# Optimization experiments

Measured on AMD Instinct MI355X. Metric: run time of the kernel, lower is better.

## Reference

```python
import jax, jax.numpy as jnp
import numpy as np
from jax import lax

EPS = 1e-5
B, T, IN, H, D = 16, 512, 128, 256, 8


def setup_inputs() -> dict:
    key = jax.random.key(0)
    ks = jax.random.split(key, 9)
    s = 0.05  # small init to keep tanh unsaturated
    f32 = jnp.float32
    return {
        "y": jax.random.normal(ks[0], (B, T, IN), f32),
        "W_ih": jax.random.normal(ks[1], (H, IN), f32) * s,
        "W_hh": jax.random.normal(ks[2], (H, H), f32) * s,
        "b_ih": jax.random.normal(ks[3], (H,), f32) * s,
        "b_hh": jax.random.normal(ks[4], (H,), f32) * s,
        "W_mean": jax.random.normal(ks[5], (D, H), f32) * s,
        "b_mean": jax.random.normal(ks[6], (D,), f32) * s,
        "W_bd": jax.random.normal(ks[7], (2 * D, H), f32) * s,
        "b_bd": jax.random.normal(ks[8], (2 * D,), f32) * s,
    }


def _forward(y, W_ih, W_hh, b_ih, b_hh, W_mean, b_mean, W_bd, b_bd):
    # --- single-layer unidirectional tanh RNN (torch nn.RNN, batch_first) ---
    x_proj = jnp.einsum("bti,hi->bth", y, W_ih) + b_ih  # [B,T,H]

    def step(h, xt):
        h_new = jnp.tanh(xt + h @ W_hh.T + b_hh)
        return h_new, h_new

    h0 = jnp.zeros((y.shape[0], W_hh.shape[0]), y.dtype)
    _, hs = lax.scan(step, h0, jnp.swapaxes(x_proj, 0, 1))  # [T,B,H]
    enc = jnp.swapaxes(hs, 0, 1)  # [B,T,H]

    mean = enc @ W_mean.T + b_mean  # [B,T,D]
    bd = enc @ W_bd.T + b_bd        # [B,T,2D]

    d = mean.shape[-1]
    t = bd.shape[1]
    diag_e = bd[:, :, :d]        # [B,T,D]  main-diag factor elems
    off_e = bd[:, :-1, d:]       # [B,T-1,D] super-diag factor elems

    a2 = diag_e ** 2
    b2 = jnp.concatenate([jnp.zeros_like(off_e[:, :1]), off_e ** 2], axis=1)  # [B,T,D]
    ab = diag_e[:, :-1] * off_e  # [B,T-1,D]

    main = jnp.swapaxes(a2 + b2, 1, 2) + EPS  # [B,D,T]  (eps*I folded into diag)
    supd = jnp.swapaxes(ab, 1, 2)             # [B,D,T-1]

    i = jnp.arange(t)
    j = jnp.arange(t - 1)
    prec = jnp.zeros((bd.shape[0], d, t, t), bd.dtype)  # [B,D,T,T]
    prec = prec.at[:, :, i, i].set(main)
    prec = prec.at[:, :, j, j + 1].set(supd)
    prec = prec.at[:, :, j + 1, j].set(supd)
    return mean, prec


def reference(y, W_ih, W_hh, b_ih, b_hh, W_mean, b_mean, W_bd, b_bd):
    # Returns the parameters of the D per-dim MultivariateNormal posteriors:
    # mean [B,T,D] and tridiagonal precision matrices [B,D,T,T].
    return _forward(y, W_ih, W_hh, b_ih, b_hh, W_mean, b_mean, W_bd, b_bd)
```

## Files before the change

kernel.cpp:

```cpp
#include <hip/hip_runtime.h>
#include <math.h>

#define BB 16
#define TT 512
#define IND 128
#define HH 256
#define DD 8
#define EPSF 1e-5f

typedef _Float16 h2_t __attribute__((ext_vector_type(2)));
typedef float f32x4 __attribute__((ext_vector_type(4)));

__device__ __forceinline__ float fast_tanh(float x) {
    x = fminf(fmaxf(x, -15.f), 15.f);
    const float e = __expf(2.f * x);
    return __fdividef(e - 1.f, e + 1.f);
}

__device__ __forceinline__ float dpp_xor1(float x) {
    int i = __builtin_bit_cast(int, x);
    i = __builtin_amdgcn_update_dpp(i, i, 0xB1, 0xF, 0xF, true);
    return __builtin_bit_cast(float, i);
}
__device__ __forceinline__ float dpp_xor2(float x) {
    int i = __builtin_bit_cast(int, x);
    i = __builtin_amdgcn_update_dpp(i, i, 0x4E, 0xF, 0xF, true);
    return __builtin_bit_cast(float, i);
}

__global__ __launch_bounds__(512, 4) void xproj_kernel(
    const float* __restrict__ y, const float* __restrict__ W_ih,
    const float* __restrict__ b_ih, const float* __restrict__ b_hh,
    float* __restrict__ xp)
{
    __shared__ __align__(16) float ylds[IND];
    const int tid = threadIdx.x;
    const int j = tid >> 1;
    const int k4 = (tid & 1) * 4;

    float4 w[16];
    const float* wr = W_ih + (size_t)j * IND + k4;
#pragma unroll
    for (int i = 0; i < 16; ++i) w[i] = *(const float4*)(wr + i * 8);
#pragma unroll
    for (int i = 0; i < 16; ++i)
        asm volatile("" : "+v"(w[i].x), "+v"(w[i].y), "+v"(w[i].z), "+v"(w[i].w));
    const float bias = b_ih[j] + b_hh[j];

    const int row0 = blockIdx.x * 16;
    for (int r = 0; r < 16; ++r) {
        const int row = row0 + r;
        if (tid < IND / 4) ((float4*)ylds)[tid] = ((const float4*)(y + (size_t)row * IND))[tid];
        __syncthreads();
        float a0 = 0.f, a1 = 0.f, a2 = 0.f, a3 = 0.f;
#pragma unroll
        for (int i = 0; i < 16; ++i) {
            const float4 hv = *(const float4*)(ylds + i * 8 + k4);
            a0 = fmaf(hv.x, w[i].x, a0);
            a1 = fmaf(hv.y, w[i].y, a1);
            a2 = fmaf(hv.z, w[i].z, a2);
            a3 = fmaf(hv.w, w[i].w, a3);
        }
        float acc = (a0 + a1) + (a2 + a3);
        acc += __shfl_xor(acc, 1);
        if ((tid & 1) == 0) xp[(size_t)row * HH + j] = acc + bias;
        __syncthreads();
    }
}

__global__ __launch_bounds__(512, 2) void scan_fill_kernel(
    const float* __restrict__ xp, const float* __restrict__ W_hh,
    float* __restrict__ enc, float* __restrict__ prec)
{
    if (blockIdx.x >= BB) {
        const size_t n4 = (size_t)BB * DD * TT * TT / 4;
        const f32x4 z = {0.f, 0.f, 0.f, 0.f};
        f32x4* p4 = (f32x4*)prec;
        size_t idx = (size_t)(blockIdx.x - BB) * blockDim.x + threadIdx.x;
        const size_t stride = (size_t)(gridDim.x - BB) * blockDim.x;
        for (; idx < n4; idx += stride) p4[idx] = z;
        return;
    }

    const int b   = blockIdx.x;
    const int tid = threadIdx.x;
    const int g   = tid >> 3;
    const int k   = tid & 7;
    const int kk  = k & 3;
    const int jw  = g + 64 * kk;
    const bool act = (k < 4);

    __shared__ __align__(16) char hbufA[4 * 144];
    __shared__ __align__(16) char hbufB[4 * 144];

    h2_t w[4][16];
#pragma unroll
    for (int m = 0; m < 4; ++m) {
        const float* wr = W_hh + (size_t)(g + 64 * m) * HH + (size_t)k * 32;
#pragma unroll
        for (int i = 0; i < 16; ++i) {
            h2_t v;
            v.x = (_Float16)wr[2 * i];
            v.y = (_Float16)wr[2 * i + 1];
            w[m][i] = v;
        }
    }
#pragma unroll
    for (int m = 0; m < 4; ++m)
#pragma unroll
        for (int i = 0; i < 16; ++i) {
            int tmp = __builtin_bit_cast(int, w[m][i]);
            asm volatile("" : "+v"(tmp));
            w[m][i] = __builtin_bit_cast(h2_t, tmp);
        }

    if (tid < 128) {
        const int m = 2 * tid;
        h2_t z; z.x = (_Float16)0.f; z.y = (_Float16)0.f;
        *(h2_t*)(hbufA + (m >> 6) * 144 + (m & 63) * 2) = z;
    }

    const float* xpb  = xp  + (size_t)b * TT * HH;
    float*       encb = enc + (size_t)b * TT * HH;

    float xbuf[4];
#pragma unroll
    for (int s = 0; s < 4; ++s) xbuf[s] = xpb[(size_t)s * HH + jw];

    __syncthreads();

    const char* hrd = hbufA;
    char* hwr = hbufB;

#define SCAN_STEP(TSTEP, S)                                                       \
    {                                                                             \
        const int t_ = (TSTEP);                                                   \
        const float xc = xbuf[S];                                                 \
        const int tp_ = (t_ + 4 < TT) ? t_ + 4 : TT - 1;                          \
        xbuf[S] = xpb[(size_t)tp_ * HH + jw];                                     \
        float a0 = 0.f, a1 = 0.f, a2 = 0.f, a3 = 0.f;                             \
        const float4* hp = (const float4*)(hrd + (k >> 1) * 144 + (k & 1) * 64);  \
        _Pragma("unroll")                                                         \
        for (int i = 0; i < 4; ++i) {                                             \
            union { float4 f4; h2_t h[4]; } u;                                    \
            u.f4 = hp[i];                                                         \
            _Pragma("unroll")                                                     \
            for (int e = 0; e < 4; ++e) {                                         \
                a0 = __builtin_amdgcn_fdot2(u.h[e], w[0][4 * i + e], a0, false);  \
                a1 = __builtin_amdgcn_fdot2(u.h[e], w[1][4 * i + e], a1, false);  \
                a2 = __builtin_amdgcn_fdot2(u.h[e], w[2][4 * i + e], a2, false);  \
                a3 = __builtin_amdgcn_fdot2(u.h[e], w[3][4 * i + e], a3, false);  \
            }                                                                     \
        }                                                                         \
        a0 += dpp_xor1(a0); a0 += dpp_xor2(a0); a0 += __shfl_xor(a0, 4);          \
        a1 += dpp_xor1(a1); a1 += dpp_xor2(a1); a1 += __shfl_xor(a1, 4);          \
        a2 += dpp_xor1(a2); a2 += dpp_xor2(a2); a2 += __shfl_xor(a2, 4);          \
        a3 += dpp_xor1(a3); a3 += dpp_xor2(a3); a3 += __shfl_xor(a3, 4);          \
        const float p = (kk & 1) ? ((kk & 2) ? a3 : a1) : ((kk & 2) ? a2 : a0);   \
        const float hn = fast_tanh(xc + p);                                       \
        if (act) {                                                                \
            encb[(size_t)t_ * HH + jw] = hn;                                      \
            *(_Float16*)(hwr + kk * 144 + g * 2) = (_Float16)hn;                  \
        }                                                                         \
        asm volatile("s_waitcnt lgkmcnt(0)\n\ts_barrier" ::: "memory");           \
        { const char* tmp_ = hrd; hrd = hwr; hwr = (char*)tmp_; }                 \
    }

    for (int tb = 0; tb < TT; tb += 4) {
        SCAN_STEP(tb,     0)
        SCAN_STEP(tb + 1, 1)
        SCAN_STEP(tb + 2, 2)
        SCAN_STEP(tb + 3, 3)
    }
#undef SCAN_STEP
}

__global__ __launch_bounds__(256) void head_kernel(
    const float* __restrict__ enc,
    const float* __restrict__ W_mean, const float* __restrict__ b_mean,
    const float* __restrict__ W_bd, const float* __restrict__ b_bd,
    float* __restrict__ mean_out, float* __restrict__ prec)
{
    const int b = blockIdx.x >> 6;
    const int t0 = (blockIdx.x & 63) * 8;
    __shared__ __align__(16) float erow[9][HH];
    __shared__ float vals[8][32];

    const int tid = threadIdx.x;
    {
        const float4* src = (const float4*)(enc + ((size_t)b * TT + t0) * HH - HH);
        float4* dst = (float4*)erow;
        for (int i = tid; i < 9 * (HH / 4); i += 256) dst[i] = src[i];
    }

    const int g = tid >> 3, m = tid & 7;
    const float* wrow;
    float bias;
    if (g < 8)       { wrow = W_mean + (size_t)g * HH;      bias = b_mean[g]; }
    else if (g < 24) { wrow = W_bd + (size_t)(g - 8) * HH;  bias = b_bd[g - 8]; }
    else             { wrow = W_bd + (size_t)(g - 16) * HH; bias = b_bd[g - 16]; }

    float4 wv[8];
#pragma unroll
    for (int i = 0; i < 8; ++i) wv[i] = ((const float4*)wrow)[m * 8 + i];

    __syncthreads();

    for (int r = 0; r < 8; ++r) {
        const float* src = (g >= 24) ? erow[r] : erow[r + 1];
        float acc = 0.f;
#pragma unroll
        for (int i = 0; i < 8; ++i) {
            const float4 hv = ((const float4*)src)[m * 8 + i];
            acc += wv[i].x * hv.x + wv[i].y * hv.y + wv[i].z * hv.z + wv[i].w * hv.w;
        }
        acc += __shfl_xor(acc, 1);
        acc += __shfl_xor(acc, 2);
        acc += __shfl_xor(acc, 4);
        if (m == 0) vals[r][g] = acc + bias;
    }
    __syncthreads();

    const int r = tid >> 5, s = tid & 31;
    const int t = t0 + r;
    if (s < DD) {
        mean_out[((size_t)b * TT + t) * DD + s] = vals[r][s];
    } else if (s < 2 * DD) {
        const int d = s - DD;
        const float diag = vals[r][8 + d];
        const float off  = vals[r][16 + d];
        const float offp = (t > 0) ? vals[r][24 + d] : 0.f;
        const size_t rowbase = (((size_t)b * DD + d) * TT + t) * TT;
        prec[rowbase + t] = diag * diag + offp * offp + EPSF;
        if (t < TT - 1) {
            const float sv = diag * off;
            prec[rowbase + t + 1] = sv;
            prec[(((size_t)b * DD + d) * TT + (t + 1)) * TT + t] = sv;
        }
    }
}

extern "C" void kernel_launch(void* const* d_in, const int* in_sizes, int n_in,
                              void* d_out, int out_size, void* d_ws, size_t ws_size,
                              hipStream_t stream) {
    const float* y      = (const float*)d_in[0];
    const float* W_ih   = (const float*)d_in[1];
    const float* W_hh   = (const float*)d_in[2];
    const float* b_ih   = (const float*)d_in[3];
    const float* b_hh   = (const float*)d_in[4];
    const float* W_mean = (const float*)d_in[5];
    const float* b_mean = (const float*)d_in[6];
    const float* W_bd   = (const float*)d_in[7];
    const float* b_bd   = (const float*)d_in[8];

    float* out  = (float*)d_out;
    float* mean = out;
    float* prec = out + (size_t)BB * TT * DD;

    float* xp  = (float*)d_ws;
    float* enc = xp + (size_t)BB * TT * HH;

    xproj_kernel<<<512, 512, 0, stream>>>(y, W_ih, b_ih, b_hh, xp);
    scan_fill_kernel<<<1008, 512, 0, stream>>>(xp, W_hh, enc, prec);
    head_kernel<<<1024, 256, 0, stream>>>(enc, W_mean, b_mean, W_bd, b_bd, mean, prec);
}
```

Before: 459.5 us.

## Halve scan block to 256 threads with 64-wide K slices per lane

Restructures the recurrent scan so each block uses 256 threads, each holding 128 fp16-pair weights over a 64-element K slice. This removes the idle half of the lanes and the cross-lane shuffle-by-4 reduction from the serial per-step critical path. The xproj kernel now stages all 16 input rows in LDS once instead of syncing per row. Smaller changes swap shuffles for DPP and drop the tanh clamp. The scan's register pressure rises sharply and the zero-fill blocks also shrink to 256 threads, which may slow the prec memset.

```diff
diff --git a/kernel.cpp b/kernel.cpp
--- a/kernel.cpp
+++ b/kernel.cpp
@@ -12,9 +12,8 @@
 typedef float f32x4 __attribute__((ext_vector_type(4)));
 
 __device__ __forceinline__ float fast_tanh(float x) {
-    x = fminf(fmaxf(x, -15.f), 15.f);
     const float e = __expf(2.f * x);
-    return __fdividef(e - 1.f, e + 1.f);
+    return 1.f - __fdividef(2.f, e + 1.f);
 }
 
 __device__ __forceinline__ float dpp_xor1(float x) {
@@ -33,7 +32,7 @@
     const float* __restrict__ b_ih, const float* __restrict__ b_hh,
     float* __restrict__ xp)
 {
-    __shared__ __align__(16) float ylds[IND];
+    __shared__ __align__(16) float ylds[16 * IND];
     const int tid = threadIdx.x;
     const int j = tid >> 1;
     const int k4 = (tid & 1) * 4;
@@ -48,27 +47,28 @@
     const float bias = b_ih[j] + b_hh[j];
 
     const int row0 = blockIdx.x * 16;
+    ((float4*)ylds)[tid] = ((const float4*)(y + (size_t)row0 * IND))[tid];
+    __syncthreads();
+
+#pragma unroll 4
     for (int r = 0; r < 16; ++r) {
-        const int row = row0 + r;
-        if (tid < IND / 4) ((float4*)ylds)[tid] = ((const float4*)(y + (size_t)row * IND))[tid];
-        __syncthreads();
+        const float* yr = ylds + r * IND + k4;
         float a0 = 0.f, a1 = 0.f, a2 = 0.f, a3 = 0.f;
 #pragma unroll
         for (int i = 0; i < 16; ++i) {
-            const float4 hv = *(const float4*)(ylds + i * 8 + k4);
+            const float4 hv = *(const float4*)(yr + i * 8);
             a0 = fmaf(hv.x, w[i].x, a0);
             a1 = fmaf(hv.y, w[i].y, a1);
             a2 = fmaf(hv.z, w[i].z, a2);
             a3 = fmaf(hv.w, w[i].w, a3);
         }
         float acc = (a0 + a1) + (a2 + a3);
-        acc += __shfl_xor(acc, 1);
-        if ((tid & 1) == 0) xp[(size_t)row * HH + j] = acc + bias;
-        __syncthreads();
-    }
-}
-
-__global__ __launch_bounds__(512, 2) void scan_fill_kernel(
+        acc += dpp_xor1(acc);
+        if ((tid & 1) == 0) xp[(size_t)(row0 + r) * HH + j] = acc + bias;
+    }
+}
+
+__global__ __launch_bounds__(256, 2) void scan_fill_kernel(
     const float* __restrict__ xp, const float* __restrict__ W_hh,
     float* __restrict__ enc, float* __restrict__ prec)
 {
@@ -84,21 +84,19 @@
 
     const int b   = blockIdx.x;
     const int tid = threadIdx.x;
-    const int g   = tid >> 3;
-    const int k   = tid & 7;
-    const int kk  = k & 3;
-    const int jw  = g + 64 * kk;
-    const bool act = (k < 4);
+    const int j0  = tid >> 2;
+    const int k   = tid & 3;
+    const int jw  = j0 + 64 * k;
 
     __shared__ __align__(16) char hbufA[4 * 144];
     __shared__ __align__(16) char hbufB[4 * 144];
 
-    h2_t w[4][16];
+    h2_t w[4][32];
 #pragma unroll
     for (int m = 0; m < 4; ++m) {
-        const float* wr = W_hh + (size_t)(g + 64 * m) * HH + (size_t)k * 32;
-#pragma unroll
-        for (int i = 0; i < 16; ++i) {
+        const float* wr = W_hh + (size_t)(j0 + 64 * m) * HH + (size_t)k * 64;
+#pragma unroll
+        for (int i = 0; i < 32; ++i) {
             h2_t v;
             v.x = (_Float16)wr[2 * i];
             v.y = (_Float16)wr[2 * i + 1];
@@ -108,7 +106,7 @@
 #pragma unroll
     for (int m = 0; m < 4; ++m)
 #pragma unroll
-        for (int i = 0; i < 16; ++i) {
+        for (int i = 0; i < 32; ++i) {
             int tmp = __builtin_bit_cast(int, w[m][i]);
             asm volatile("" : "+v"(tmp));
             w[m][i] = __builtin_bit_cast(h2_t, tmp);
@@ -121,57 +119,63 @@
     }
 
     const float* xpb  = xp  + (size_t)b * TT * HH;
-    float*       encb = enc + (size_t)b * TT * HH;
 
     float xbuf[4];
 #pragma unroll
     for (int s = 0; s < 4; ++s) xbuf[s] = xpb[(size_t)s * HH + jw];
+    const float* xpf = xpb + (size_t)4 * HH + jw;
+    float*      encp = enc + (size_t)b * TT * HH + jw;
+
+    const int roff = k * 144;
+    const int hoff = k * 144 + j0 * 2;
 
     __syncthreads();
 
     const char* hrd = hbufA;
     char* hwr = hbufB;
 
-#define SCAN_STEP(TSTEP, S)                                                       \
+#define SCAN_STEP(S, PF)                                                          \
     {                                                                             \
-        const int t_ = (TSTEP);                                                   \
         const float xc = xbuf[S];                                                 \
-        const int tp_ = (t_ + 4 < TT) ? t_ + 4 : TT - 1;                          \
-        xbuf[S] = xpb[(size_t)tp_ * HH + jw];                                     \
+        if (PF) xbuf[S] = xpf[(S) * HH];                                          \
         float a0 = 0.f, a1 = 0.f, a2 = 0.f, a3 = 0.f;                             \
-        const float4* hp = (const float4*)(hrd + (k >> 1) * 144 + (k & 1) * 64);  \
+        const float4* hp = (const float4*)(hrd + roff);                           \
         _Pragma("unroll")                                                         \
-        for (int i = 0; i < 4; ++i) {                                             \
+        for (int i = 0; i < 8; ++i) {                                             \
             union { float4 f4; h2_t h[4]; } u;                                    \
             u.f4 = hp[i];                                                         \
             _Pragma("unroll")                                                     \
-            for (int e = 0; e < 4; ++e) {                                         \
-                a0 = __builtin_amdgcn_fdot2(u.h[e], w[0][4 * i + e], a0, false);  \
-                a1 = __builtin_amdgcn_fdot2(u.h[e], w[1][4 * i + e], a1, false);  \
-                a2 = __builtin_amdgcn_fdot2(u.h[e], w[2][4 * i + e], a2, false);  \
-                a3 = __builtin_amdgcn_fdot2(u.h[e], w[3][4 * i + e], a3, false);  \
+            for (int q = 0; q < 4; ++q) {                                         \
+                a0 = __builtin_amdgcn_fdot2(u.h[q], w[0][4 * i + q], a0, false);  \
+                a1 = __builtin_amdgcn_fdot2(u.h[q], w[1][4 * i + q], a1, false);  \
+                a2 = __builtin_amdgcn_fdot2(u.h[q], w[2][4 * i + q], a2, false);  \
+                a3 = __builtin_amdgcn_fdot2(u.h[q], w[3][4 * i + q], a3, false);  \
             }                                                                     \
         }                                                                         \
-        a0 += dpp_xor1(a0); a0 += dpp_xor2(a0); a0 += __shfl_xor(a0, 4);          \
-        a1 += dpp_xor1(a1); a1 += dpp_xor2(a1); a1 += __shfl_xor(a1, 4);          \
-        a2 += dpp_xor1(a2); a2 += dpp_xor2(a2); a2 += __shfl_xor(a2, 4);          \
-        a3 += dpp_xor1(a3); a3 += dpp_xor2(a3); a3 += __shfl_xor(a3, 4);          \
-        const float p = (kk & 1) ? ((kk & 2) ? a3 : a1) : ((kk & 2) ? a2 : a0);   \
+        a0 += dpp_xor1(a0); a0 += dpp_xor2(a0);                                   \
+        a1 += dpp_xor1(a1); a1 += dpp_xor2(a1);                                   \
+        a2 += dpp_xor1(a2); a2 += dpp_xor2(a2);                                   \
+        a3 += dpp_xor1(a3); a3 += dpp_xor2(a3);                                   \
+        const float p = (k & 1) ? ((k & 2) ? a3 : a1) : ((k & 2) ? a2 : a0);      \
         const float hn = fast_tanh(xc + p);                                       \
-        if (act) {                                                                \
-            encb[(size_t)t_ * HH + jw] = hn;                                      \
-            *(_Float16*)(hwr + kk * 144 + g * 2) = (_Float16)hn;                  \
-        }                                                                         \
+        encp[(S) * HH] = hn;                                                      \
+        *(_Float16*)(hwr + hoff) = (_Float16)hn;                                  \
         asm volatile("s_waitcnt lgkmcnt(0)\n\ts_barrier" ::: "memory");           \
         { const char* tmp_ = hrd; hrd = hwr; hwr = (char*)tmp_; }                 \
     }
 
-    for (int tb = 0; tb < TT; tb += 4) {
-        SCAN_STEP(tb,     0)
-        SCAN_STEP(tb + 1, 1)
-        SCAN_STEP(tb + 2, 2)
-        SCAN_STEP(tb + 3, 3)
-    }
+    for (int tb = 0; tb < TT - 4; tb += 4) {
+        SCAN_STEP(0, 1)
+        SCAN_STEP(1, 1)
+        SCAN_STEP(2, 1)
+        SCAN_STEP(3, 1)
+        xpf  += 4 * HH;
+        encp += 4 * HH;
+    }
+    SCAN_STEP(0, 0)
+    SCAN_STEP(1, 0)
+    SCAN_STEP(2, 0)
+    SCAN_STEP(3, 0)
 #undef SCAN_STEP
 }
 
@@ -214,8 +218,8 @@
             const float4 hv = ((const float4*)src)[m * 8 + i];
             acc += wv[i].x * hv.x + wv[i].y * hv.y + wv[i].z * hv.z + wv[i].w * hv.w;
         }
-        acc += __shfl_xor(acc, 1);
-        acc += __shfl_xor(acc, 2);
+        acc += dpp_xor1(acc);
+        acc += dpp_xor2(acc);
         acc += __shfl_xor(acc, 4);
         if (m == 0) vals[r][g] = acc + bias;
     }
@@ -261,6 +265,6 @@
     float* enc = xp + (size_t)BB * TT * HH;
 
     xproj_kernel<<<512, 512, 0, stream>>>(y, W_ih, b_ih, b_hh, xp);
-    scan_fill_kernel<<<1008, 512, 0, stream>>>(xp, W_hh, enc, prec);
+    scan_fill_kernel<<<1008, 256, 0, stream>>>(xp, W_hh, enc, prec);
     head_kernel<<<1024, 256, 0, stream>>>(enc, W_mean, b_mean, W_bd, b_bd, mean, prec);
 }
```

New measurement: 407.5 us, median of 2. 11.3% less time.
